# Optimization experiments

Hardware: AMD Instinct MI355X
Metric: run time of the kernel (lower is better)

Reference implementation:

```python
import jax, jax.numpy as jnp
import numpy as np

NEG_INF = -1e30  # stand-in for -inf padding in TF SAME maxpool


def setup_inputs() -> dict:
    key = jax.random.key(0)
    x = jax.random.normal(key, (16, 8192, 256), dtype=jnp.float32)
    # Fixed (non-trainable) kernels exactly as in build()
    blur = np.array([2.0, 4.0, 2.0], dtype=np.float32)
    blur = blur / blur.sum()
    blur_kernel = jnp.asarray(blur.reshape(3, 1, 1))
    avg_kernel = jnp.asarray(np.array([0.5, 0.5], dtype=np.float32).reshape(2, 1, 1))
    return {"x": x, "blur_kernel": blur_kernel, "avg_kernel": avg_kernel}


def reference(x, blur_kernel, avg_kernel):
    # x: [B, L, C] (NWC). Equivalent to the per-channel loop, vectorized over C.
    B, L, C = x.shape
    # 1) Max pool, window=2, stride=1, padding SAME -> TF pads one -inf at the END.
    x_pad = jnp.pad(x, ((0, 0), (0, 1), (0, 0)), constant_values=NEG_INF)
    m = jnp.maximum(x_pad[:, :L, :], x_pad[:, 1:L + 1, :])  # [B, L, C]
    # 2) Blur conv1d kernel [.25,.5,.25], padding 'same' (zero pad 1 each side).
    b = blur_kernel[:, 0, 0]
    mp = jnp.pad(m, ((0, 0), (1, 1), (0, 0)))
    y = b[0] * mp[:, :L, :] + b[1] * mp[:, 1:L + 1, :] + b[2] * mp[:, 2:L + 2, :]
    # 3) Avg conv1d kernel [.5,.5], padding 'valid', stride 2.
    a = avg_kernel[:, 0, 0]
    z = a[0] * y[:, 0:L - 1:2, :] + a[1] * y[:, 1:L:2, :]  # [B, L//2, C]
    return z
```

## Files before the change

kernel.cpp:

```cpp
#include <hip/hip_runtime.h>

static constexpr int B     = 16;
static constexpr int L     = 8192;
static constexpr int C     = 256;
static constexpr int C4    = C / 4;
static constexpr int LOUT  = L / 2;
static constexpr int JPT   = 16;
static constexpr int CHUNKS = LOUT / JPT;

__device__ __forceinline__ float4 f4max(float4 a, float4 b) {
    return make_float4(fmaxf(a.x, b.x), fmaxf(a.y, b.y),
                       fmaxf(a.z, b.z), fmaxf(a.w, b.w));
}

__global__ __launch_bounds__(256) void maxblurpool_kernel(
    const float4* __restrict__ x,
    const float*  __restrict__ blur,
    const float*  __restrict__ avg,
    float4*       __restrict__ out)
{
    const int tid   = blockIdx.x * 256 + threadIdx.x;
    const int c4    = tid & (C4 - 1);
    const int col   = tid >> 6;
    const int chunk = col & (CHUNKS - 1);
    const int b     = col >> 8;

    const float b0 = blur[0], b1 = blur[1], b2 = blur[2];
    const float a0 = avg[0],  a1 = avg[1];
    const float w0 = a0 * b0;
    const float w1 = a0 * b1 + a1 * b0;
    const float w2 = a0 * b2 + a1 * b1;
    const float w3 = a1 * b2;

    const int  j0 = chunk * JPT;
    const long l0 = 2L * j0;
    const float4* xp = x   + (long)b * L    * C4 + c4;
    float4*       op = out + (long)b * LOUT * C4 + c4;

    float4 x_cur  = xp[l0 * C4];
    float4 x_last = xp[(l0 + 1) * C4];
    float4 m_prev;
    if (j0 == 0) {
        m_prev = make_float4(0.f, 0.f, 0.f, 0.f);
    } else {
        float4 x_prev = xp[(l0 - 1) * C4];
        m_prev = f4max(x_prev, x_cur);
    }
    float4 m_cur = f4max(x_cur, x_last);

    #pragma unroll
    for (int jj = 0; jj < JPT; ++jj) {
        const int  j  = j0 + jj;
        const long l2 = 2L * j + 2;
        float4 m1, m2, xb;
        if (l2 < L) {
            float4 xa = xp[l2 * C4];
            xb        = xp[(l2 + 1) * C4];
            m1 = f4max(x_last, xa);
            m2 = f4max(xa, xb);
        } else {
            m1 = x_last;
            m2 = make_float4(0.f, 0.f, 0.f, 0.f);
            xb = m2;
        }
        float4 z;
        z.x = w0 * m_prev.x + w1 * m_cur.x + w2 * m1.x + w3 * m2.x;
        z.y = w0 * m_prev.y + w1 * m_cur.y + w2 * m1.y + w3 * m2.y;
        z.z = w0 * m_prev.z + w1 * m_cur.z + w2 * m1.z + w3 * m2.z;
        z.w = w0 * m_prev.w + w1 * m_cur.w + w2 * m1.w + w3 * m2.w;
        op[(long)j * C4] = z;
        m_prev = m1; m_cur = m2; x_last = xb;
    }
}

extern "C" void kernel_launch(void* const* d_in, const int* in_sizes, int n_in,
                              void* d_out, int out_size, void* d_ws, size_t ws_size,
                              hipStream_t stream) {
    const float4* x    = (const float4*)d_in[0];
    const float*  blur = (const float*)d_in[1];
    const float*  avg  = (const float*)d_in[2];
    float4*       out  = (float4*)d_out;

    const int total_threads = B * CHUNKS * C4;
    const int block = 256;
    const int grid  = total_threads / block;
    maxblurpool_kernel<<<grid, block, 0, stream>>>(x, blur, avg, out);
}
```

Baseline: 213.3 us.

## Preload all input rows per thread, halve chunk size, swizzle blocks, nontemporal stores

```diff
diff --git a/kernel.cpp b/kernel.cpp
--- a/kernel.cpp
+++ b/kernel.cpp
@@ -1,12 +1,15 @@
 #include <hip/hip_runtime.h>
 
-static constexpr int B     = 16;
-static constexpr int L     = 8192;
-static constexpr int C     = 256;
-static constexpr int C4    = C / 4;
-static constexpr int LOUT  = L / 2;
-static constexpr int JPT   = 16;
-static constexpr int CHUNKS = LOUT / JPT;
+static constexpr int B    = 16;
+static constexpr int L    = 8192;
+static constexpr int C    = 256;
+static constexpr int C4   = C / 4;
+static constexpr int LOUT = L / 2;
+static constexpr int JPT  = 8;
+static constexpr int QPB  = LOUT / JPT;
+static constexpr int NROW = 2 * JPT + 3;
+
+typedef float vfloat4 __attribute__((ext_vector_type(4)));
 
 __device__ __forceinline__ float4 f4max(float4 a, float4 b) {
     return make_float4(fmaxf(a.x, b.x), fmaxf(a.y, b.y),
@@ -19,11 +22,16 @@
     const float*  __restrict__ avg,
     float4*       __restrict__ out)
 {
-    const int tid   = blockIdx.x * 256 + threadIdx.x;
-    const int c4    = tid & (C4 - 1);
-    const int col   = tid >> 6;
-    const int chunk = col & (CHUNKS - 1);
-    const int b     = col >> 8;
+    const int nblk    = gridDim.x;
+    const int hw      = blockIdx.x;
+    const int logical = (hw & 7) * (nblk >> 3) + (hw >> 3);
+
+    const int lane = threadIdx.x & 63;
+    const int wib  = threadIdx.x >> 6;
+    const int q    = logical * 4 + wib;
+    const int b    = q >> 9;
+    const int j0   = (q & (QPB - 1)) * JPT;
+    const int i0   = 2 * j0 - 1;
 
     const float b0 = blur[0], b1 = blur[1], b2 = blur[2];
     const float a0 = avg[0],  a1 = avg[1];
@@ -32,44 +40,33 @@
     const float w2 = a0 * b2 + a1 * b1;
     const float w3 = a1 * b2;
 
-    const int  j0 = chunk * JPT;
-    const long l0 = 2L * j0;
-    const float4* xp = x   + (long)b * L    * C4 + c4;
-    float4*       op = out + (long)b * LOUT * C4 + c4;
+    const float4* xp = x   + (long)b * L    * C4 + lane;
+    float4*       op = out + (long)b * LOUT * C4 + lane;
 
-    float4 x_cur  = xp[l0 * C4];
-    float4 x_last = xp[(l0 + 1) * C4];
-    float4 m_prev;
-    if (j0 == 0) {
-        m_prev = make_float4(0.f, 0.f, 0.f, 0.f);
-    } else {
-        float4 x_prev = xp[(l0 - 1) * C4];
-        m_prev = f4max(x_prev, x_cur);
+    float4 xr[NROW];
+    #pragma unroll
+    for (int k = 0; k < NROW; ++k) {
+        int r = i0 + k;
+        r = r < 0 ? 0 : (r > L - 1 ? L - 1 : r);
+        xr[k] = xp[(long)r * C4];
     }
-    float4 m_cur = f4max(x_cur, x_last);
+
+    float4 m[NROW - 1];
+    #pragma unroll
+    for (int k = 0; k < NROW - 1; ++k) m[k] = f4max(xr[k], xr[k + 1]);
 
     #pragma unroll
-    for (int jj = 0; jj < JPT; ++jj) {
-        const int  j  = j0 + jj;
-        const long l2 = 2L * j + 2;
-        float4 m1, m2, xb;
-        if (l2 < L) {
-            float4 xa = xp[l2 * C4];
-            xb        = xp[(l2 + 1) * C4];
-            m1 = f4max(x_last, xa);
-            m2 = f4max(xa, xb);
-        } else {
-            m1 = x_last;
-            m2 = make_float4(0.f, 0.f, 0.f, 0.f);
-            xb = m2;
-        }
-        float4 z;
-        z.x = w0 * m_prev.x + w1 * m_cur.x + w2 * m1.x + w3 * m2.x;
-        z.y = w0 * m_prev.y + w1 * m_cur.y + w2 * m1.y + w3 * m2.y;
-        z.z = w0 * m_prev.z + w1 * m_cur.z + w2 * m1.z + w3 * m2.z;
-        z.w = w0 * m_prev.w + w1 * m_cur.w + w2 * m1.w + w3 * m2.w;
-        op[(long)j * C4] = z;
-        m_prev = m1; m_cur = m2; x_last = xb;
+    for (int t = 0; t < JPT; ++t) {
+        const float W0 = (t == 0        && j0 == 0)           ? 0.f : w0;
+        const float W3 = (t == JPT - 1  && j0 == LOUT - JPT)  ? 0.f : w3;
+        const float4 ma = m[2 * t], mb = m[2 * t + 1];
+        const float4 mc = m[2 * t + 2], md = m[2 * t + 3];
+        vfloat4 z;
+        z.x = W0 * ma.x + w1 * mb.x + w2 * mc.x + W3 * md.x;
+        z.y = W0 * ma.y + w1 * mb.y + w2 * mc.y + W3 * md.y;
+        z.z = W0 * ma.z + w1 * mb.z + w2 * mc.z + W3 * md.z;
+        z.w = W0 * ma.w + w1 * mb.w + w2 * mc.w + W3 * md.w;
+        __builtin_nontemporal_store(z, (vfloat4*)&op[(long)(j0 + t) * C4]);
     }
 }
 
@@ -81,7 +78,7 @@
     const float*  avg  = (const float*)d_in[2];
     float4*       out  = (float4*)d_out;
 
-    const int total_threads = B * CHUNKS * C4;
+    const int total_threads = B * QPB * C4;
     const int block = 256;
     const int grid  = total_threads / block;
     maxblurpool_kernel<<<grid, block, 0, stream>>>(x, blur, avg, out);
```

After: 219.6 us. +2.9%, slower.
